# Kernel optimization log

Measured on AMD Instinct MI355X. Metric: run time of the kernel, lower is better.

The kernel has to match this reference:

```python
import jax, jax.numpy as jnp
import numpy as np

V, E, H, B, T = 50000, 300, 150, 64, 512  # vocab, embed_dim, hidden_dim, batch, seq_len
ATTN = H // 2


def setup_inputs() -> dict:
    key = jax.random.key(0)
    ks = jax.random.split(key, 18)
    s = 0.08
    inp = {
        "texts": jax.random.randint(ks[0], (B, T), 0, V, dtype=jnp.int32),
        "lengths": jax.random.randint(ks[1], (B,), 1, T + 1, dtype=jnp.int32),
        "emb_table": jax.random.normal(ks[2], (V, E), jnp.float32) * s,
        # layer 0 GRU (torch gate order: reset | update | new)
        "Wih0": jax.random.normal(ks[3], (3 * H, E), jnp.float32) * s,
        "Whh0": jax.random.normal(ks[4], (3 * H, H), jnp.float32) * s,
        "bih0": jax.random.normal(ks[5], (3 * H,), jnp.float32) * s,
        "bhh0": jax.random.normal(ks[6], (3 * H,), jnp.float32) * s,
        # layer 1 GRU
        "Wih1": jax.random.normal(ks[7], (3 * H, H), jnp.float32) * s,
        "Whh1": jax.random.normal(ks[8], (3 * H, H), jnp.float32) * s,
        "bih1": jax.random.normal(ks[9], (3 * H,), jnp.float32) * s,
        "bhh1": jax.random.normal(ks[10], (3 * H,), jnp.float32) * s,
        # additive attention
        "W1": jax.random.normal(ks[11], (ATTN, H), jnp.float32) * s,
        "w2": jax.random.normal(ks[12], (1, ATTN), jnp.float32) * s,
        # classifier head
        "fc1_w": jax.random.normal(ks[13], (H, H), jnp.float32) * s,
        "fc1_b": jax.random.normal(ks[14], (H,), jnp.float32) * s,
        "fc2_w": jax.random.normal(ks[15], (1, H), jnp.float32) * s,
        "fc2_b": jax.random.normal(ks[16], (1,), jnp.float32) * s,
    }
    return inp


def _gru_layer(x, Wih, Whh, bih, bhh, mask):
    # x: [T, B, I]; mask: [T, B, 1] True where t < length (packed-sequence semantics)
    h0 = jnp.zeros((x.shape[1], Whh.shape[1]), x.dtype)
    xw = x @ Wih.T + bih  # precompute input projections for all steps: [T, B, 3H]

    def step(h, inp):
        xw_t, m = inp
        hg = h @ Whh.T + bhh
        xr, xz, xn = jnp.split(xw_t, 3, axis=-1)
        hr, hz, hn = jnp.split(hg, 3, axis=-1)
        r = jax.nn.sigmoid(xr + hr)
        z = jax.nn.sigmoid(xz + hz)
        n = jnp.tanh(xn + r * hn)
        h_new = (1.0 - z) * n + z * h
        h_next = jnp.where(m, h_new, h)        # hidden freezes past length
        out = jnp.where(m, h_new, 0.0)          # pad_packed_sequence pads with zeros
        return h_next, out

    h_last, outs = jax.lax.scan(step, h0, (xw, mask))
    return outs, h_last


def reference(texts, lengths, emb_table, Wih0, Whh0, bih0, bhh0,
              Wih1, Whh1, bih1, bhh1, W1, w2, fc1_w, fc1_b, fc2_w, fc2_b):
    emb = emb_table[texts]                    # [B, T, E]
    x = jnp.transpose(emb, (1, 0, 2))         # [T, B, E] (batch_first=False)
    t_idx = jnp.arange(x.shape[0], dtype=lengths.dtype)
    mask = (t_idx[:, None] < lengths[None, :])[:, :, None]  # [T, B, 1]

    out0, _ = _gru_layer(x, Wih0, Whh0, bih0, bhh0, mask)
    out1, _ = _gru_layer(out0, Wih1, Whh1, bih1, bhh1, mask)  # [T, B, H]

    # additive attention over time (unmasked softmax, matching the original)
    scores = (jnp.tanh(out1 @ W1.T) @ w2.T)[..., 0].T        # [B, T]
    attn = jax.nn.softmax(scores, axis=1)                    # [B, T]
    ctx = jnp.einsum('bt,tbh->bh', attn, out1)               # [B, H]

    hcls = jax.nn.relu(ctx @ fc1_w.T + fc1_b)
    logits = (hcls @ fc2_w.T + fc2_b)[:, 0]                  # [B]
    return logits
```

## Files before the change

kernel.cpp:

```cpp
#include <hip/hip_runtime.h>

#define TT 512
#define BB 64
#define EE 300
#define HH 150
#define G3 450
#define AT 75

typedef float v2f __attribute__((ext_vector_type(2)));

__device__ __forceinline__ float fast_rcp(float x) { return __builtin_amdgcn_rcpf(x); }
__device__ __forceinline__ float sigmoid_f(float x) { return fast_rcp(1.f + __expf(-x)); }
__device__ __forceinline__ float tanh_f(float x) {
  float e = __expf(2.f * x);
  return 1.f - 2.f * fast_rcp(e + 1.f);
}

__global__ void k_prep(const float* __restrict__ Wih0, const float* __restrict__ Whh0,
                       const float* __restrict__ Wih1, const float* __restrict__ Whh1,
                       const float* __restrict__ W1,   const float* __restrict__ fc1w,
                       float* __restrict__ Wih0T, float* __restrict__ Whh0T,
                       float* __restrict__ Wih1T, float* __restrict__ Whh1T,
                       float* __restrict__ W1T,   float* __restrict__ fc1T) {
  int tid = blockIdx.x * blockDim.x + threadIdx.x;
  int nt = gridDim.x * blockDim.x;
  for (int i = tid; i < G3 * EE; i += nt) { int r = i / EE, c = i - r * EE; Wih0T[c * G3 + r] = Wih0[i]; }
  for (int i = tid; i < G3 * HH; i += nt) { int r = i / HH, c = i - r * HH; Whh0T[c * G3 + r] = Whh0[i]; }
  for (int i = tid; i < G3 * HH; i += nt) { int r = i / HH, c = i - r * HH; Wih1T[c * G3 + r] = Wih1[i]; }
  for (int i = tid; i < G3 * HH; i += nt) { int r = i / HH, c = i - r * HH; Whh1T[c * G3 + r] = Whh1[i]; }
  for (int i = tid; i < AT * HH; i += nt) { int r = i / HH, c = i - r * HH; W1T[c * AT + r] = W1[i]; }
  for (int i = tid; i < HH * HH; i += nt) { int r = i / HH, c = i - r * HH; fc1T[c * HH + r] = fc1w[i]; }
}

__global__ __launch_bounds__(512) void k_xw0(const int* __restrict__ texts,
                                             const float* __restrict__ emb,
                                             const float* __restrict__ WihT,
                                             const float* __restrict__ bih,
                                             float* __restrict__ xw) {
  __shared__ __align__(16) float a_lds[32 * EE];
  const int row0 = blockIdx.x * 32;
  const int tid = threadIdx.x;
  for (int p = tid; p < 32 * EE; p += 512) {
    int r = p / EE, e = p - r * EE;
    int vrow = texts[row0 + r];
    a_lds[p] = emb[(size_t)vrow * EE + e];
  }
  __syncthreads();
  const int g = tid;
  if (g < G3) {
    float acc[32];
#pragma unroll
    for (int r = 0; r < 32; ++r) acc[r] = 0.f;
    const float bias = bih[g];
    for (int k = 0; k < EE; k += 4) {
      float w0 = WihT[(k + 0) * G3 + g];
      float w1 = WihT[(k + 1) * G3 + g];
      float w2v = WihT[(k + 2) * G3 + g];
      float w3 = WihT[(k + 3) * G3 + g];
#pragma unroll
      for (int r = 0; r < 32; ++r) {
        const float4 av = *reinterpret_cast<const float4*>(&a_lds[r * EE + k]);
        acc[r] = fmaf(av.x, w0, acc[r]);
        acc[r] = fmaf(av.y, w1, acc[r]);
        acc[r] = fmaf(av.z, w2v, acc[r]);
        acc[r] = fmaf(av.w, w3, acc[r]);
      }
    }
#pragma unroll
    for (int r = 0; r < 32; ++r) xw[(size_t)(row0 + r) * G3 + g] = acc[r] + bias;
  }
}

__global__ __launch_bounds__(512) void k_xw1(const float* __restrict__ in,
                                             const float* __restrict__ WihT,
                                             const float* __restrict__ bih,
                                             float* __restrict__ xw) {
  __shared__ __align__(16) float a_lds[32 * 152];
  const int row0 = blockIdx.x * 32;
  const int tid = threadIdx.x;
  for (int p = tid; p < 32 * HH; p += 512) {
    int r = p / HH, e = p - r * HH;
    a_lds[r * 152 + e] = in[(size_t)(row0 + r) * HH + e];
  }
  __syncthreads();
  const int g = tid;
  if (g < G3) {
    float acc[32];
#pragma unroll
    for (int r = 0; r < 32; ++r) acc[r] = 0.f;
    const float bias = bih[g];
    for (int k = 0; k < 148; k += 4) {
      float w0 = WihT[(k + 0) * G3 + g];
      float w1 = WihT[(k + 1) * G3 + g];
      float w2v = WihT[(k + 2) * G3 + g];
      float w3 = WihT[(k + 3) * G3 + g];
#pragma unroll
      for (int r = 0; r < 32; ++r) {
        const float4 av = *reinterpret_cast<const float4*>(&a_lds[r * 152 + k]);
        acc[r] = fmaf(av.x, w0, acc[r]);
        acc[r] = fmaf(av.y, w1, acc[r]);
        acc[r] = fmaf(av.z, w2v, acc[r]);
        acc[r] = fmaf(av.w, w3, acc[r]);
      }
    }
    {
      float w0 = WihT[148 * G3 + g];
      float w1 = WihT[149 * G3 + g];
#pragma unroll
      for (int r = 0; r < 32; ++r) {
        acc[r] = fmaf(a_lds[r * 152 + 148], w0, acc[r]);
        acc[r] = fmaf(a_lds[r * 152 + 149], w1, acc[r]);
      }
    }
#pragma unroll
    for (int r = 0; r < 32; ++r) xw[(size_t)(row0 + r) * G3 + g] = acc[r] + bias;
  }
}

__global__ __launch_bounds__(512, 2) void k_rec(const float* __restrict__ WhhT,
                                                const float* __restrict__ bhh,
                                                const float* __restrict__ xw,
                                                const int* __restrict__ lengths,
                                                float* __restrict__ out) {
  const int b = blockIdx.x;
  const int tid = threadIdx.x;
  __shared__ __align__(16) float h_lds[152];
  __shared__ float hg_lds[G3];
  const int len = lengths[b];

  const bool active = tid < G3;
  const int g = active ? tid : 0;

  v2f w[75];
#pragma unroll
  for (int k = 0; k < 75; ++k) {
    w[k][0] = WhhT[(2 * k) * G3 + g];
    w[k][1] = WhhT[(2 * k + 1) * G3 + g];
  }
#pragma unroll
  for (int k = 0; k < 75; ++k) asm volatile("" : "+v"(w[k]));

  const float bias = bhh[g];
  if (tid < 152) h_lds[tid] = 0.f;
  float h_reg = 0.f;
  __syncthreads();

  const float* xwb = xw + (size_t)b * TT * G3;
  float* outb = out + (size_t)b * TT * HH;
  const float4* h4 = reinterpret_cast<const float4*>(h_lds);

  for (int t = 0; t < len; ++t) {
    float xr = 0.f, xz = 0.f, xn = 0.f;
    if (tid < HH) {
      const float* xwt = xwb + (size_t)t * G3;
      xr = xwt[tid]; xz = xwt[tid + HH]; xn = xwt[tid + 2 * HH];
    }
    v2f a0 = {0.f, 0.f}, a1 = {0.f, 0.f};
#pragma unroll
    for (int q = 0; q < 37; ++q) {
      const float4 hv = h4[q];
      v2f hx = {hv.x, hv.y};
      v2f hy = {hv.z, hv.w};
      a0 = __builtin_elementwise_fma(w[2 * q], hx, a0);
      a1 = __builtin_elementwise_fma(w[2 * q + 1], hy, a1);
    }
    {
      const float4 hv = h4[37];
      v2f hx = {hv.x, hv.y};
      a0 = __builtin_elementwise_fma(w[74], hx, a0);
    }
    if (active) hg_lds[g] = bias + (a0[0] + a1[0]) + (a0[1] + a1[1]);
    __syncthreads();

    if (tid < HH) {
      const float hr = hg_lds[tid], hz = hg_lds[tid + HH], hn = hg_lds[tid + 2 * HH];
      const float r = sigmoid_f(xr + hr);
      const float z = sigmoid_f(xz + hz);
      const float n = tanh_f(xn + r * hn);
      const float hnew = (1.f - z) * n + z * h_reg;
      h_reg = hnew;
      h_lds[tid] = hnew;
      outb[(size_t)t * HH + tid] = hnew;
    }
    __syncthreads();
  }
  const int rem = (TT - len) * HH;
  float* outp = outb + (size_t)len * HH;
  for (int p = tid; p < rem; p += 512) outp[p] = 0.f;
}

__global__ __launch_bounds__(256) void k_scores(const float* __restrict__ out1,
                                                const float* __restrict__ W1T,
                                                const float* __restrict__ w2,
                                                float* __restrict__ scores) {
  const int row0 = blockIdx.x * 32;
  const int tid = threadIdx.x;
  __shared__ float sc[32];
  if (tid < 32) sc[tid] = 0.f;
  __syncthreads();
  for (int p = tid; p < 32 * AT; p += 256) {
    const int r = p / AT, a = p - r * AT;
    const float* x = out1 + (size_t)(row0 + r) * HH;
    float a0 = 0.f, a1 = 0.f;
    for (int k = 0; k < HH; k += 2) {
      a0 = fmaf(W1T[k * AT + a], x[k], a0);
      a1 = fmaf(W1T[(k + 1) * AT + a], x[k + 1], a1);
    }
    atomicAdd(&sc[r], tanh_f(a0 + a1) * w2[a]);
  }
  __syncthreads();
  if (tid < 32) scores[row0 + tid] = sc[tid];
}

__global__ __launch_bounds__(512) void k_final(const float* __restrict__ out1,
                                               const float* __restrict__ scores,
                                               const float* __restrict__ fc1T,
                                               const float* __restrict__ fc1b,
                                               const float* __restrict__ fc2w,
                                               const float* __restrict__ fc2b,
                                               float* __restrict__ logits) {
  const int b = blockIdx.x;
  const int tid = threadIdx.x;
  __shared__ float attn[TT];
  __shared__ float red[16];
  __shared__ float ctx[152];
  __shared__ float h1[152];

  float s = scores[b * TT + tid];
  float m = s;
#pragma unroll
  for (int off = 32; off > 0; off >>= 1) m = fmaxf(m, __shfl_xor(m, off));
  const int wave = tid >> 6;
  if ((tid & 63) == 0) red[wave] = m;
  __syncthreads();
  if (tid == 0) {
    float mm = red[0];
#pragma unroll
    for (int i = 1; i < 8; ++i) mm = fmaxf(mm, red[i]);
    red[8] = mm;
  }
  __syncthreads();
  const float mx = red[8];
  const float e = __expf(s - mx);
  attn[tid] = e;
  float zz = e;
#pragma unroll
  for (int off = 32; off > 0; off >>= 1) zz += __shfl_xor(zz, off);
  if ((tid & 63) == 0) red[wave] = zz;
  __syncthreads();
  if (tid == 0) {
    float ss = 0.f;
#pragma unroll
    for (int i = 0; i < 8; ++i) ss += red[i];
    red[9] = ss;
  }
  __syncthreads();
  const float invZ = 1.f / red[9];

  if (tid < HH) {
    const float* o1b = out1 + (size_t)b * TT * HH;
    float c0 = 0.f, c1 = 0.f, c2 = 0.f, c3 = 0.f;
    for (int t = 0; t < TT; t += 4) {
      c0 = fmaf(attn[t + 0], o1b[(t + 0) * HH + tid], c0);
      c1 = fmaf(attn[t + 1], o1b[(t + 1) * HH + tid], c1);
      c2 = fmaf(attn[t + 2], o1b[(t + 2) * HH + tid], c2);
      c3 = fmaf(attn[t + 3], o1b[(t + 3) * HH + tid], c3);
    }
    ctx[tid] = ((c0 + c1) + (c2 + c3)) * invZ;
  }
  __syncthreads();
  if (tid < HH) {
    float d0 = 0.f, d1 = 0.f;
    for (int k = 0; k < HH; k += 2) {
      d0 = fmaf(fc1T[k * HH + tid], ctx[k], d0);
      d1 = fmaf(fc1T[(k + 1) * HH + tid], ctx[k + 1], d1);
    }
    h1[tid] = fmaxf(d0 + d1 + fc1b[tid], 0.f);
  }
  __syncthreads();
  if (tid == 0) {
    float acc = fc2b[0];
    for (int k = 0; k < HH; ++k) acc = fmaf(fc2w[k], h1[k], acc);
    logits[b] = acc;
  }
}

extern "C" void kernel_launch(void* const* d_in, const int* in_sizes, int n_in,
                              void* d_out, int out_size, void* d_ws, size_t ws_size,
                              hipStream_t stream) {
  const int* texts     = (const int*)d_in[0];
  const int* lengths   = (const int*)d_in[1];
  const float* emb     = (const float*)d_in[2];
  const float* Wih0    = (const float*)d_in[3];
  const float* Whh0    = (const float*)d_in[4];
  const float* bih0    = (const float*)d_in[5];
  const float* bhh0    = (const float*)d_in[6];
  const float* Wih1    = (const float*)d_in[7];
  const float* Whh1    = (const float*)d_in[8];
  const float* bih1    = (const float*)d_in[9];
  const float* bhh1    = (const float*)d_in[10];
  const float* W1      = (const float*)d_in[11];
  const float* w2      = (const float*)d_in[12];
  const float* fc1w    = (const float*)d_in[13];
  const float* fc1b    = (const float*)d_in[14];
  const float* fc2w    = (const float*)d_in[15];
  const float* fc2b    = (const float*)d_in[16];
  float* logits = (float*)d_out;

  float* ws = (float*)d_ws;
  size_t off = 0;
  auto alloc = [&](size_t n) { float* p = ws + off; off += (n + 3) & ~(size_t)3; return p; };
  float* Wih0T  = alloc((size_t)G3 * EE);
  float* Whh0T  = alloc((size_t)G3 * HH);
  float* Wih1T  = alloc((size_t)G3 * HH);
  float* Whh1T  = alloc((size_t)G3 * HH);
  float* W1T    = alloc((size_t)AT * HH);
  float* fc1T   = alloc((size_t)HH * HH);
  float* xwbuf  = alloc((size_t)BB * TT * G3);
  float* out0   = alloc((size_t)BB * TT * HH);
  float* out1   = alloc((size_t)BB * TT * HH);
  float* scores = alloc((size_t)BB * TT);
  (void)ws_size; (void)in_sizes; (void)n_in; (void)out_size;

  hipLaunchKernelGGL(k_prep, dim3(256), dim3(256), 0, stream,
                     Wih0, Whh0, Wih1, Whh1, W1, fc1w,
                     Wih0T, Whh0T, Wih1T, Whh1T, W1T, fc1T);
  hipLaunchKernelGGL(k_xw0, dim3((BB * TT) / 32), dim3(512), 0, stream, texts, emb, Wih0T, bih0, xwbuf);
  hipLaunchKernelGGL(k_rec, dim3(BB), dim3(512), 0, stream, Whh0T, bhh0, xwbuf, lengths, out0);
  hipLaunchKernelGGL(k_xw1, dim3((BB * TT) / 32), dim3(512), 0, stream, out0, Wih1T, bih1, xwbuf);
  hipLaunchKernelGGL(k_rec, dim3(BB), dim3(512), 0, stream, Whh1T, bhh1, xwbuf, lengths, out1);
  hipLaunchKernelGGL(k_scores, dim3((BB * TT) / 32), dim3(256), 0, stream, out1, W1T, w2, scores);
  hipLaunchKernelGGL(k_final, dim3(BB), dim3(512), 0, stream, out1, scores, fc1T, fc1b, fc2w, fc2b, logits);
}
```

Baseline: 1.291 ms.

## Split GRU recurrent matvec over K across three thread groups per step

The recurrent kernel's work is re-partitioned. Before, each of 450 threads computed one gate row over all 150 hidden inputs. Now three groups of 150 threads each compute all three gates (r, z, n) for one hidden unit over a third of the K range, and the partial sums are reduced through shared memory by the first group. This cuts per-thread shared-memory reads of h and the serial dependency length in each timestep. In exchange it adds zero-padded FMAs, extra shared-memory partial stores and loads, and keeps three gates' weights in registers per thread.

```diff
diff --git a/kernel.cpp b/kernel.cpp
--- a/kernel.cpp
+++ b/kernel.cpp
@@ -6,6 +6,7 @@
 #define HH 150
 #define G3 450
 #define AT 75
+#define NW 28
 
 typedef float v2f __attribute__((ext_vector_type(2)));
 
@@ -125,23 +126,33 @@
   const int b = blockIdx.x;
   const int tid = threadIdx.x;
   __shared__ __align__(16) float h_lds[152];
-  __shared__ float hg_lds[G3];
+  __shared__ float part[2][G3 + 6];
   const int len = lengths[b];
 
-  const bool active = tid < G3;
-  const int g = active ? tid : 0;
-
-  v2f w[75];
-#pragma unroll
-  for (int k = 0; k < 75; ++k) {
-    w[k][0] = WhhT[(2 * k) * G3 + g];
-    w[k][1] = WhhT[(2 * k + 1) * G3 + g];
-  }
-#pragma unroll
-  for (int k = 0; k < 75; ++k) asm volatile("" : "+v"(w[k]));
-
-  const float bias = bhh[g];
-  if (tid < 152) h_lds[tid] = 0.f;
+  int g = tid / 150;
+  const bool worker = g < 3;
+  const int gg = worker ? g : 2;
+  const int j = worker ? (tid - 150 * g) : 0;
+  const int kreal_end = (gg == 2) ? 150 : 48 * (gg + 1);
+  const int h4base = 12 * gg;
+
+  v2f w[3][NW];
+#pragma unroll
+  for (int r = 0; r < 3; ++r) {
+    const int row = j + 150 * r;
+#pragma unroll
+    for (int q = 0; q < NW; ++q) {
+      const int k0 = 48 * gg + 2 * q;
+      const int k1 = k0 + 1;
+      w[r][q][0] = (worker && k0 < kreal_end) ? WhhT[k0 * G3 + row] : 0.f;
+      w[r][q][1] = (worker && k1 < kreal_end) ? WhhT[k1 * G3 + row] : 0.f;
+    }
+  }
+  const float bias_r = bhh[j];
+  const float bias_z = bhh[j + 150];
+  const float bias_n = bhh[j + 300];
+
+  for (int p = tid; p < 152; p += 512) h_lds[p] = 0.f;
   float h_reg = 0.f;
   __syncthreads();
 
@@ -155,25 +166,35 @@
       const float* xwt = xwb + (size_t)t * G3;
       xr = xwt[tid]; xz = xwt[tid + HH]; xn = xwt[tid + 2 * HH];
     }
-    v2f a0 = {0.f, 0.f}, a1 = {0.f, 0.f};
-#pragma unroll
-    for (int q = 0; q < 37; ++q) {
-      const float4 hv = h4[q];
-      v2f hx = {hv.x, hv.y};
-      v2f hy = {hv.z, hv.w};
-      a0 = __builtin_elementwise_fma(w[2 * q], hx, a0);
-      a1 = __builtin_elementwise_fma(w[2 * q + 1], hy, a1);
-    }
-    {
-      const float4 hv = h4[37];
-      v2f hx = {hv.x, hv.y};
-      a0 = __builtin_elementwise_fma(w[74], hx, a0);
-    }
-    if (active) hg_lds[g] = bias + (a0[0] + a1[0]) + (a0[1] + a1[1]);
+    v2f ar0 = {0.f, 0.f}, ar1 = {0.f, 0.f};
+    v2f az0 = {0.f, 0.f}, az1 = {0.f, 0.f};
+    v2f an0 = {0.f, 0.f}, an1 = {0.f, 0.f};
+#pragma unroll
+    for (int q = 0; q < 14; ++q) {
+      const float4 hv = h4[h4base + q];
+      const v2f hx = {hv.x, hv.y};
+      const v2f hy = {hv.z, hv.w};
+      ar0 = __builtin_elementwise_fma(w[0][2 * q],     hx, ar0);
+      ar1 = __builtin_elementwise_fma(w[0][2 * q + 1], hy, ar1);
+      az0 = __builtin_elementwise_fma(w[1][2 * q],     hx, az0);
+      az1 = __builtin_elementwise_fma(w[1][2 * q + 1], hy, az1);
+      an0 = __builtin_elementwise_fma(w[2][2 * q],     hx, an0);
+      an1 = __builtin_elementwise_fma(w[2][2 * q + 1], hy, an1);
+    }
+    const float pr = (ar0[0] + ar0[1]) + (ar1[0] + ar1[1]);
+    const float pz = (az0[0] + az0[1]) + (az1[0] + az1[1]);
+    const float pn = (an0[0] + an0[1]) + (an1[0] + an1[1]);
+    if (worker && g > 0) {
+      part[g - 1][j] = pr;
+      part[g - 1][j + 150] = pz;
+      part[g - 1][j + 300] = pn;
+    }
     __syncthreads();
 
     if (tid < HH) {
-      const float hr = hg_lds[tid], hz = hg_lds[tid + HH], hn = hg_lds[tid + 2 * HH];
+      const float hr = pr + part[0][tid] + part[1][tid] + bias_r;
+      const float hz = pz + part[0][tid + 150] + part[1][tid + 150] + bias_z;
+      const float hn = pn + part[0][tid + 300] + part[1][tid + 300] + bias_n;
       const float r = sigmoid_f(xr + hr);
       const float z = sigmoid_f(xz + hz);
       const float n = tanh_f(xn + r * hn);
```

New measurement: 1.139 ms. -11.8%, faster.
